# Kernel tuning notes

Measured on AMD Instinct MI355X. Metric: run time of the kernel, lower is better.

## Reference

```python
import jax, jax.numpy as jnp
import numpy as np

EPS_W = 1e-8   # weight reciprocal eps (matches torch code)
EPS_BN = 1e-5  # torch BatchNorm1d default eps


def _cdist(a, b):
    # a: [B,N,3], b: [B,M,3] -> [B,N,M] euclidean distances
    sq = (jnp.sum(a * a, -1)[:, :, None] + jnp.sum(b * b, -1)[:, None, :]
          - 2.0 * jnp.einsum('bnd,bmd->bnm', a, b))
    return jnp.sqrt(jnp.maximum(sq, 0.0))


def _bn_relu(x, gamma, beta):
    # x: [B,C,N]; training-mode batch norm over (B,N)
    mean = jnp.mean(x, axis=(0, 2), keepdims=True)
    var = jnp.mean((x - mean) ** 2, axis=(0, 2), keepdims=True)
    y = (x - mean) * jax.lax.rsqrt(var + EPS_BN)
    y = y * gamma[None, :, None] + beta[None, :, None]
    return jax.nn.relu(y)


def setup_inputs() -> dict:
    key = jax.random.key(0)
    ks = jax.random.split(key, 8)
    B, Np, Ns = 16, 1024, 4096
    Cp, Cs, Co = 256, 128, 256
    return {
        'xyz_prev': jax.random.normal(ks[0], (B, Np, 3), jnp.float32),
        'xyz_skip': jax.random.normal(ks[1], (B, Ns, 3), jnp.float32),
        'points_prev': jax.random.normal(ks[2], (B, Cp, Np), jnp.float32),
        'points_skip': jax.random.normal(ks[3], (B, Cs, Ns), jnp.float32),
        'W1': jax.random.normal(ks[4], (Co, Cp + Cs), jnp.float32) * 0.05,
        'g1': jnp.ones((Co,), jnp.float32),
        'b1': jnp.zeros((Co,), jnp.float32),
        'W2': jax.random.normal(ks[5], (Co, Co), jnp.float32) * 0.05,
        'g2': jnp.ones((Co,), jnp.float32),
        'b2': jnp.zeros((Co,), jnp.float32),
    }


def reference(xyz_prev, xyz_skip, points_prev, points_skip, W1, g1, b1, W2, g2, b2):
    dist = _cdist(xyz_skip, xyz_prev)                       # [B,Ns,Np]
    neg, idx = jax.lax.top_k(-dist, 3)                      # 3 smallest dists
    dist_recip = 1.0 / (dist + EPS_W)
    # NOTE: normalization is over ALL N_prev points (faithful to source)
    weight = dist_recip / jnp.sum(dist_recip, axis=2, keepdims=True)
    w3 = jnp.take_along_axis(weight, idx, axis=2)           # [B,Ns,3]
    pp = jnp.swapaxes(points_prev, 1, 2)                    # [B,Np,Cp]
    g = jnp.take_along_axis(pp[:, None, :, :], idx[..., None], axis=2)  # [B,Ns,3,Cp]
    interp = jnp.einsum('bnk,bnkc->bcn', w3, g)             # [B,Cp,Ns]
    x = jnp.concatenate([interp, points_skip], axis=1)      # [B,Cp+Cs,Ns]
    x = _bn_relu(jnp.einsum('bcn,oc->bon', x, W1), g1, b1)
    x = _bn_relu(jnp.einsum('bcn,oc->bon', x, W2), g2, b2)
    return x
```

## Files before the change

kernel.cpp:

```cpp
#include <hip/hip_runtime.h>
#include <math.h>

constexpr int NB  = 16;
constexpr int NP  = 1024;
constexpr int NS  = 4096;
constexpr int CP  = 256;
constexpr int CS  = 128;
constexpr int CIN = 384;
constexpr int CO  = 256;

constexpr int NCHUNK = 16;
constexpr int CHPTS  = NP / NCHUNK;

typedef unsigned int uint;
typedef unsigned short ushort_t;
typedef __attribute__((ext_vector_type(8))) short short8;
typedef __attribute__((ext_vector_type(4))) float f32x4;

__device__ __forceinline__ ushort_t f2bf(float f) {
  uint u = __float_as_uint(f);
  uint r = (u + 0x7fffu + ((u >> 16) & 1u)) >> 16;
  return (ushort_t)r;
}
__device__ __forceinline__ float bf2f(ushort_t u) {
  return __uint_as_float(((uint)u) << 16);
}
__device__ __forceinline__ uint pk2(ushort_t lo, ushort_t hi) {
  return (uint)lo | ((uint)hi << 16);
}

__device__ __forceinline__ void gload16(const void* g, void* l) {
  __builtin_amdgcn_global_load_lds(
      (const __attribute__((address_space(1))) uint*)g,
      (__attribute__((address_space(3))) uint*)l, 16, 0, 0);
}

__device__ __forceinline__ void tkp(float pxv, float pyv, float pzv, int pi,
                                    float qx, float qy, float qz,
                                    float& k0, float& k1, float& k2,
                                    float& rsum) {
  float dx = pxv - qx, dy = pyv - qy, dz = pzv - qz;
  float sq = fmaf(dz, dz, fmaf(dy, dy, fmaf(dx, dx, 1e-16f)));
  rsum += __builtin_amdgcn_rsqf(sq);
  float k = __uint_as_float((__float_as_uint(sq) & 0xFFFFFC00u) | (uint)pi);
  k2 = __builtin_amdgcn_fmed3f(k1, k2, k);
  k1 = __builtin_amdgcn_fmed3f(k0, k1, k);
  k0 = fminf(k0, k);
}

__global__ __launch_bounds__(256) void topk_chunk_kernel(
    const float* __restrict__ xyz_prev, const float* __restrict__ xyz_skip,
    float* __restrict__ pbuf) {
  __shared__ float px[CHPTS], py[CHPTS], pz[CHPTS];
  int q  = blockIdx.y;
  int b  = blockIdx.z;
  int tid = threadIdx.x;
  if (tid < CHPTS) {
    const float* xp = xyz_prev + ((size_t)b * NP + q * CHPTS + tid) * 3;
    px[tid] = xp[0]; py[tid] = xp[1]; pz[tid] = xp[2];
  }
  __syncthreads();
  int nA = blockIdx.x * 512 + tid;
  int nB = nA + 256;
  const float* xqA = xyz_skip + ((size_t)b * NS + nA) * 3;
  const float* xqB = xyz_skip + ((size_t)b * NS + nB) * 3;
  float qxA = xqA[0], qyA = xqA[1], qzA = xqA[2];
  float qxB = xqB[0], qyB = xqB[1], qzB = xqB[2];
  float kA0 = INFINITY, kA1 = INFINITY, kA2 = INFINITY;
  float kB0 = INFINITY, kB1 = INFINITY, kB2 = INFINITY;
  float rsA = 0.f, rsB = 0.f;
  int pbase = q * CHPTS;

  for (int p = 0; p < CHPTS; p += 4) {
    float4 X = *(const float4*)&px[p];
    float4 Y = *(const float4*)&py[p];
    float4 Z = *(const float4*)&pz[p];
    tkp(X.x, Y.x, Z.x, pbase + p + 0, qxA, qyA, qzA, kA0, kA1, kA2, rsA);
    tkp(X.x, Y.x, Z.x, pbase + p + 0, qxB, qyB, qzB, kB0, kB1, kB2, rsB);
    tkp(X.y, Y.y, Z.y, pbase + p + 1, qxA, qyA, qzA, kA0, kA1, kA2, rsA);
    tkp(X.y, Y.y, Z.y, pbase + p + 1, qxB, qyB, qzB, kB0, kB1, kB2, rsB);
    tkp(X.z, Y.z, Z.z, pbase + p + 2, qxA, qyA, qzA, kA0, kA1, kA2, rsA);
    tkp(X.z, Y.z, Z.z, pbase + p + 2, qxB, qyB, qzB, kB0, kB1, kB2, rsB);
    tkp(X.w, Y.w, Z.w, pbase + p + 3, qxA, qyA, qzA, kA0, kA1, kA2, rsA);
    tkp(X.w, Y.w, Z.w, pbase + p + 3, qxB, qyB, qzB, kB0, kB1, kB2, rsB);
  }

  size_t PA = ((size_t)(b * NCHUNK + q) * NS + nA) * 4;
  size_t PB = ((size_t)(b * NCHUNK + q) * NS + nB) * 4;
  *(float4*)(pbuf + PA) = make_float4(kA0, kA1, kA2, rsA);
  *(float4*)(pbuf + PB) = make_float4(kB0, kB1, kB2, rsB);
}

__global__ __launch_bounds__(256) void topk_merge_kernel(
    const float* __restrict__ pbuf, float* __restrict__ w3,
    int* __restrict__ idx3) {
  int gid = blockIdx.x * 256 + threadIdx.x;
  int b = gid >> 12;
  int n = gid & (NS - 1);
  float k0 = INFINITY, k1 = INFINITY, k2 = INFINITY;
  float rsum = 0.f;
  #pragma unroll 4
  for (int q = 0; q < NCHUNK; q++) {
    float4 v = *(const float4*)(pbuf + ((size_t)(b * NCHUNK + q) * NS + n) * 4);
    rsum += v.w;
    k2 = __builtin_amdgcn_fmed3f(k1, k2, v.x);
    k1 = __builtin_amdgcn_fmed3f(k0, k1, v.x);
    k0 = fminf(k0, v.x);
    k2 = __builtin_amdgcn_fmed3f(k1, k2, v.y);
    k1 = __builtin_amdgcn_fmed3f(k0, k1, v.y);
    k0 = fminf(k0, v.y);
    k2 = __builtin_amdgcn_fmed3f(k1, k2, v.z);
    k1 = __builtin_amdgcn_fmed3f(k0, k1, v.z);
    k0 = fminf(k0, v.z);
  }
  float inv = 1.0f / rsum;
  uint u0 = __float_as_uint(k0), u1 = __float_as_uint(k1), u2 = __float_as_uint(k2);
  float d0 = __uint_as_float(u0 & 0xFFFFFC00u);
  float d1 = __uint_as_float(u1 & 0xFFFFFC00u);
  float d2 = __uint_as_float(u2 & 0xFFFFFC00u);
  size_t base = (size_t)gid * 3;
  w3[base + 0] = __builtin_amdgcn_rsqf(d0) * inv;
  w3[base + 1] = __builtin_amdgcn_rsqf(d1) * inv;
  w3[base + 2] = __builtin_amdgcn_rsqf(d2) * inv;
  idx3[base + 0] = (int)(u0 & 1023u);
  idx3[base + 1] = (int)(u1 & 1023u);
  idx3[base + 2] = (int)(u2 & 1023u);
}

__global__ __launch_bounds__(256) void wcast_kernel(
    const float* __restrict__ W1, const float* __restrict__ W2,
    ushort_t* __restrict__ W1b, ushort_t* __restrict__ W2b,
    float* __restrict__ st1, float* __restrict__ st2) {
  int tid = threadIdx.x;
  if (blockIdx.x == 0) {
    st1[tid] = 0.f; st1[tid + 256] = 0.f;
    st2[tid] = 0.f; st2[tid + 256] = 0.f;
  }
  int t = blockIdx.x * 256 + tid;
  int n1 = CO * CIN / 4;
  if (t < n1) {
    float4 v = *(const float4*)(W1 + t * 4);
    ushort4 o; o.x = f2bf(v.x); o.y = f2bf(v.y); o.z = f2bf(v.z); o.w = f2bf(v.w);
    *(ushort4*)(W1b + t * 4) = o;
  } else {
    int u = t - n1;
    float4 v = *(const float4*)(W2 + u * 4);
    ushort4 o; o.x = f2bf(v.x); o.y = f2bf(v.y); o.z = f2bf(v.z); o.w = f2bf(v.w);
    *(ushort4*)(W2b + u * 4) = o;
  }
}

__global__ __launch_bounds__(256) void ppT_kernel(
    const float* __restrict__ pp, ushort_t* __restrict__ pptT) {
  __shared__ float tl[64][65];
  int p0 = blockIdx.x * 64, c0 = blockIdx.y * 64, b = blockIdx.z;
  int tid = threadIdx.x;
  const float* P = pp + (size_t)b * CP * NP;
  int pi4 = (tid & 15) * 4, ci = tid >> 4;
  #pragma unroll
  for (int r = 0; r < 4; r++) {
    int cc = ci + 16 * r;
    float4 v = *(const float4*)(P + (size_t)(c0 + cc) * NP + p0 + pi4);
    tl[cc][pi4] = v.x; tl[cc][pi4 + 1] = v.y; tl[cc][pi4 + 2] = v.z; tl[cc][pi4 + 3] = v.w;
  }
  __syncthreads();
  ushort_t* O = pptT + (size_t)b * NP * CP;
  int ci4 = (tid & 15) * 4, pi = tid >> 4;
  #pragma unroll
  for (int r = 0; r < 4; r++) {
    int pr = pi + 16 * r;
    ushort4 o;
    o.x = f2bf(tl[ci4 + 0][pr]); o.y = f2bf(tl[ci4 + 1][pr]);
    o.z = f2bf(tl[ci4 + 2][pr]); o.w = f2bf(tl[ci4 + 3][pr]);
    *(ushort4*)(O + (size_t)(p0 + pr) * CP + c0 + ci4) = o;
  }
}

__global__ __launch_bounds__(256) void skipT_kernel(
    const float* __restrict__ sk, ushort_t* __restrict__ x1) {
  __shared__ float tl[64][65];
  int n0 = blockIdx.x * 64, c0 = blockIdx.y * 64, b = blockIdx.z;
  int tid = threadIdx.x;
  const float* S = sk + (size_t)b * CS * NS;
  int ni4 = (tid & 15) * 4, ci = tid >> 4;
  #pragma unroll
  for (int r = 0; r < 4; r++) {
    int cc = ci + 16 * r;
    float4 v = *(const float4*)(S + (size_t)(c0 + cc) * NS + n0 + ni4);
    tl[cc][ni4] = v.x; tl[cc][ni4 + 1] = v.y; tl[cc][ni4 + 2] = v.z; tl[cc][ni4 + 3] = v.w;
  }
  __syncthreads();
  ushort_t* O = x1 + (size_t)b * NS * CIN;
  int ci4 = (tid & 15) * 4, ni = tid >> 4;
  #pragma unroll
  for (int r = 0; r < 4; r++) {
    int nr = ni + 16 * r;
    ushort4 o;
    o.x = f2bf(tl[ci4 + 0][nr]); o.y = f2bf(tl[ci4 + 1][nr]);
    o.z = f2bf(tl[ci4 + 2][nr]); o.w = f2bf(tl[ci4 + 3][nr]);
    *(ushort4*)(O + (size_t)(n0 + nr) * CIN + CP + c0 + ci4) = o;
  }
}

__global__ __launch_bounds__(256) void interp_kernel(
    const ushort_t* __restrict__ pptT, const float* __restrict__ w3,
    const int* __restrict__ idx3, ushort_t* __restrict__ x1) {
  int tid = threadIdx.x;
  int nl = tid >> 6, l = tid & 63;
  int b = blockIdx.y;
  int n = blockIdx.x * 4 + nl;
  size_t nb = (size_t)b * NS + n;
  int j0 = idx3[nb * 3 + 0], j1 = idx3[nb * 3 + 1], j2 = idx3[nb * 3 + 2];
  float w0 = w3[nb * 3 + 0], w1 = w3[nb * 3 + 1], w2 = w3[nb * 3 + 2];
  const ushort_t* P = pptT + (size_t)b * NP * CP;
  int c = l * 4;
  ushort4 g0 = *(const ushort4*)(P + (size_t)j0 * CP + c);
  ushort4 g1 = *(const ushort4*)(P + (size_t)j1 * CP + c);
  ushort4 g2 = *(const ushort4*)(P + (size_t)j2 * CP + c);
  ushort4 o;
  o.x = f2bf(w0 * bf2f(g0.x) + w1 * bf2f(g1.x) + w2 * bf2f(g2.x));
  o.y = f2bf(w0 * bf2f(g0.y) + w1 * bf2f(g1.y) + w2 * bf2f(g2.y));
  o.z = f2bf(w0 * bf2f(g0.z) + w1 * bf2f(g1.z) + w2 * bf2f(g2.z));
  o.w = f2bf(w0 * bf2f(g0.w) + w1 * bf2f(g1.w) + w2 * bf2f(g2.w));
  *(ushort4*)(x1 + nb * CIN + c) = o;
}

template <int KD, bool ACT>
__global__ __launch_bounds__(256) void gemm_mfma_kernel(
    const ushort_t* __restrict__ X, const ushort_t* __restrict__ Wb,
    const float* __restrict__ stats_in, const float* __restrict__ g_in,
    const float* __restrict__ bt_in,
    ushort_t* __restrict__ Yb, float* __restrict__ stats) {
  __shared__ ushort_t ldsX[128 * 32];
  __shared__ ushort_t ldsW[128 * 32];
  __shared__ float ssum[128], ssq[128];
  __shared__ float a1s[ACT ? CO : 1], s1s[ACT ? CO : 1];
  int tid = threadIdx.x;
  int w = tid >> 6, l = tid & 63;
  int bid = blockIdx.x;
  int by = (bid >> 3) & 1;
  int s  = (bid & 7) + 8 * (bid >> 4);
  int bx = s & 31;
  int bz = s >> 5;
  int n0 = bx * 128;
  if (tid < 128) { ssum[tid] = 0.f; ssq[tid] = 0.f; }
  if constexpr (ACT) {
    float cnt = (float)NB * (float)NS;
    float m = stats_in[tid] / cnt;
    float var = stats_in[CO + tid] / cnt - m * m;
    var = fmaxf(var, 0.f);
    float invs = rsqrtf(var + 1e-5f);
    float av = g_in[tid] * invs;
    a1s[tid] = av; s1s[tid] = bt_in[tid] - m * av;
  }
  __syncthreads();

  f32x4 acc[4][4];
  #pragma unroll
  for (int i = 0; i < 4; i++)
    #pragma unroll
    for (int j = 0; j < 4; j++) acc[i][j] = {0.f, 0.f, 0.f, 0.f};

  int wn = (w & 1) * 64, wo = (w >> 1) * 64;
  int lr = l & 15, lk = l >> 4;
  const ushort_t* Xb = X + (size_t)bz * NS * KD;
  int rbase = w * 16 + (l >> 2);
  int cl = l & 3;
  int ksw = 8 * (cl ^ ((rbase >> 1) & 3));

  for (int kt = 0; kt < KD / 32; kt++) {
    int k0 = kt * 32;
    int ks = k0 + ksw;
    #pragma unroll
    for (int q = 0; q < 2; q++) {
      int r = q * 64 + rbase;
      gload16(Wb + (size_t)(by * 128 + r) * KD + ks, &ldsW[(q * 64 + w * 16) * 32]);
    }
    if constexpr (!ACT) {
      #pragma unroll
      for (int q = 0; q < 2; q++) {
        int r = q * 64 + rbase;
        gload16(Xb + (size_t)(n0 + r) * KD + ks, &ldsX[(q * 64 + w * 16) * 32]);
      }
    } else {
      float4 av0 = *(const float4*)&a1s[ks];
      float4 av1 = *(const float4*)&a1s[ks + 4];
      float4 sv0 = *(const float4*)&s1s[ks];
      float4 sv1 = *(const float4*)&s1s[ks + 4];
      #pragma unroll
      for (int q = 0; q < 2; q++) {
        int r = q * 64 + rbase;
        const ushort_t* src = Xb + (size_t)(n0 + r) * KD + ks;
        ushort4 v0 = *(const ushort4*)(src);
        ushort4 v1 = *(const ushort4*)(src + 4);
        int4 o;
        o.x = (int)pk2(f2bf(fmaxf(fmaf(av0.x, bf2f(v0.x), sv0.x), 0.f)),
                       f2bf(fmaxf(fmaf(av0.y, bf2f(v0.y), sv0.y), 0.f)));
        o.y = (int)pk2(f2bf(fmaxf(fmaf(av0.z, bf2f(v0.z), sv0.z), 0.f)),
                       f2bf(fmaxf(fmaf(av0.w, bf2f(v0.w), sv0.w), 0.f)));
        o.z = (int)pk2(f2bf(fmaxf(fmaf(av1.x, bf2f(v1.x), sv1.x), 0.f)),
                       f2bf(fmaxf(fmaf(av1.y, bf2f(v1.y), sv1.y), 0.f)));
        o.w = (int)pk2(f2bf(fmaxf(fmaf(av1.z, bf2f(v1.z), sv1.z), 0.f)),
                       f2bf(fmaxf(fmaf(av1.w, bf2f(v1.w), sv1.w), 0.f)));
        *(int4*)&ldsX[(q * 64 + w * 16) * 32 + l * 8] = o;
      }
    }
    __syncthreads();
    short8 a[4], bfr[4];
    #pragma unroll
    for (int i = 0; i < 4; i++) {
      int rr = wn + i * 16 + lr;
      int cs = lk ^ ((rr >> 1) & 3);
      a[i] = *(const short8*)&ldsX[rr * 32 + cs * 8];
    }
    #pragma unroll
    for (int j = 0; j < 4; j++) {
      int rr = wo + j * 16 + lr;
      int cs = lk ^ ((rr >> 1) & 3);
      bfr[j] = *(const short8*)&ldsW[rr * 32 + cs * 8];
    }
    #pragma unroll
    for (int i = 0; i < 4; i++)
      #pragma unroll
      for (int j = 0; j < 4; j++)
        acc[i][j] = __builtin_amdgcn_mfma_f32_16x16x32_bf16(a[i], bfr[j], acc[i][j], 0, 0, 0);
    __syncthreads();
  }

  #pragma unroll
  for (int j = 0; j < 4; j++) {
    int ol = wo + j * 16 + lr;
    int og = by * 128 + ol;
    float ps = 0.f, pq = 0.f;
    #pragma unroll
    for (int i = 0; i < 4; i++) {
      #pragma unroll
      for (int rg = 0; rg < 4; rg++) {
        float v = acc[i][j][rg];
        ps += v; pq += v * v;
        int n = n0 + wn + i * 16 + lk * 4 + rg;
        Yb[((size_t)bz * NS + n) * CO + og] = f2bf(v);
      }
    }
    atomicAdd(&ssum[ol], ps);
    atomicAdd(&ssq[ol], pq);
  }
  __syncthreads();
  if (tid < 128) {
    atomicAdd(&stats[by * 128 + tid], ssum[tid]);
    atomicAdd(&stats[CO + by * 128 + tid], ssq[tid]);
  }
}

__global__ __launch_bounds__(256) void bnrelu_tr_kernel(
    const ushort_t* __restrict__ y2b, const float* __restrict__ stats_in,
    const float* __restrict__ g_in, const float* __restrict__ bt_in,
    float* __restrict__ out) {
  __shared__ float tl[64][65];
  __shared__ float a2s[64], s2s[64];
  int n0 = blockIdx.x * 64, o0 = blockIdx.y * 64, b = blockIdx.z;
  const ushort_t* Y = y2b + (size_t)b * NS * CO;
  int tid = threadIdx.x;
  if (tid < 64) {
    int o = o0 + tid;
    float cnt = (float)NB * (float)NS;
    float m = stats_in[o] / cnt;
    float var = stats_in[CO + o] / cnt - m * m;
    var = fmaxf(var, 0.f);
    float invs = rsqrtf(var + 1e-5f);
    float av = g_in[o] * invs;
    a2s[tid] = av; s2s[tid] = bt_in[o] - m * av;
  }
  int o8 = (tid & 7) * 8, row = tid >> 3;
  #pragma unroll
  for (int r = 0; r < 2; r++) {
    int ii = row + 32 * r;
    const ushort_t* src = Y + (size_t)(n0 + ii) * CO + o0 + o8;
    ushort4 v0 = *(const ushort4*)(src);
    ushort4 v1 = *(const ushort4*)(src + 4);
    tl[ii][o8 + 0] = bf2f(v0.x); tl[ii][o8 + 1] = bf2f(v0.y);
    tl[ii][o8 + 2] = bf2f(v0.z); tl[ii][o8 + 3] = bf2f(v0.w);
    tl[ii][o8 + 4] = bf2f(v1.x); tl[ii][o8 + 5] = bf2f(v1.y);
    tl[ii][o8 + 6] = bf2f(v1.z); tl[ii][o8 + 7] = bf2f(v1.w);
  }
  __syncthreads();
  float* O = out + (size_t)b * CO * NS;
  int ii4 = (tid & 15) * 4, j = tid >> 4;
  #pragma unroll
  for (int r = 0; r < 4; r++) {
    int jj = j + 16 * r;
    float av = a2s[jj], sv = s2s[jj];
    float4 v;
    v.x = fmaxf(fmaf(av, tl[ii4 + 0][jj], sv), 0.f);
    v.y = fmaxf(fmaf(av, tl[ii4 + 1][jj], sv), 0.f);
    v.z = fmaxf(fmaf(av, tl[ii4 + 2][jj], sv), 0.f);
    v.w = fmaxf(fmaf(av, tl[ii4 + 3][jj], sv), 0.f);
    *(float4*)(O + (size_t)(o0 + jj) * NS + n0 + ii4) = v;
  }
}

extern "C" void kernel_launch(void* const* d_in, const int* in_sizes, int n_in,
                              void* d_out, int out_size, void* d_ws, size_t ws_size,
                              hipStream_t stream) {
  const float* xyz_prev    = (const float*)d_in[0];
  const float* xyz_skip    = (const float*)d_in[1];
  const float* points_prev = (const float*)d_in[2];
  const float* points_skip = (const float*)d_in[3];
  const float* W1 = (const float*)d_in[4];
  const float* g1 = (const float*)d_in[5];
  const float* b1 = (const float*)d_in[6];
  const float* W2 = (const float*)d_in[7];
  const float* g2 = (const float*)d_in[8];
  const float* b2 = (const float*)d_in[9];
  float* out = (float*)d_out;

  char* W = (char*)d_ws;
  size_t off = 0;
  auto alloc = [&](size_t bytes) {
    size_t o = off; off = (off + bytes + 255) & ~(size_t)255; return o;
  };
  ushort_t* x1   = (ushort_t*)(W + alloc((size_t)NB * NS * CIN * 2));
  ushort_t* y1b  = (ushort_t*)(W + alloc((size_t)NB * NS * CO * 2));
  ushort_t* pptT = (ushort_t*)(W + alloc((size_t)NB * NP * CP * 2));
  ushort_t* W1b  = (ushort_t*)(W + alloc((size_t)CO * CIN * 2));
  ushort_t* W2b  = (ushort_t*)(W + alloc((size_t)CO * CO * 2));
  float* w3   = (float*)(W + alloc((size_t)NB * NS * 3 * 4));
  int*   idx3 = (int*)(W + alloc((size_t)NB * NS * 3 * 4));
  float* st1  = (float*)(W + alloc(512 * 4));
  float* st2  = (float*)(W + alloc(512 * 4));
  size_t y2_off = alloc((size_t)NB * NS * CO * 2);
  bool full = (ws_size >= off);
  ushort_t* y2b = full ? (ushort_t*)(W + y2_off) : (ushort_t*)d_out;
  float* pbuf = full ? (float*)(W + y2_off) : (float*)d_out;

  hipLaunchKernelGGL(topk_chunk_kernel, dim3(NS / 512, NCHUNK, NB), dim3(256), 0,
                     stream, xyz_prev, xyz_skip, pbuf);
  hipLaunchKernelGGL(topk_merge_kernel, dim3(NB * NS / 256), dim3(256), 0, stream,
                     pbuf, w3, idx3);
  hipLaunchKernelGGL(wcast_kernel, dim3((CO * CIN / 4 + CO * CO / 4 + 255) / 256),
                     dim3(256), 0, stream, W1, W2, W1b, W2b, st1, st2);
  hipLaunchKernelGGL(ppT_kernel, dim3(NP / 64, CP / 64, NB), dim3(256), 0, stream,
                     points_prev, pptT);
  hipLaunchKernelGGL(skipT_kernel, dim3(NS / 64, CS / 64, NB), dim3(256), 0, stream,
                     points_skip, x1);
  hipLaunchKernelGGL(interp_kernel, dim3(NS / 4, NB), dim3(256), 0, stream,
                     pptT, w3, idx3, x1);
  hipLaunchKernelGGL((gemm_mfma_kernel<CIN, false>), dim3(1024), dim3(256),
                     0, stream, x1, W1b, (const float*)nullptr,
                     (const float*)nullptr, (const float*)nullptr, y1b, st1);
  hipLaunchKernelGGL((gemm_mfma_kernel<CO, true>), dim3(1024), dim3(256),
                     0, stream, y1b, W2b, st1, g1, b1, y2b, st2);
  if (full) {
    hipLaunchKernelGGL(bnrelu_tr_kernel, dim3(NS / 64, CO / 64, NB), dim3(256), 0,
                       stream, y2b, st2, g2, b2, out);
  } else {
    float* stage = (float*)d_ws;
    hipLaunchKernelGGL(bnrelu_tr_kernel, dim3(NS / 64, CO / 64, NB), dim3(256), 0,
                       stream, y2b, st2, g2, b2, stage);
    hipMemcpyAsync(out, stage, (size_t)NB * NS * CO * 4, hipMemcpyDeviceToDevice,
                   stream);
  }
}
```

Before: 157.9 us.

## Fuse interpolation gather into first GEMM and pipeline operand loads

Removes the separate interp kernel: the first GEMM now gathers three neighbour rows from the transposed prev features, blends them with the weights in registers and writes the bf16 tile into LDS. Skip features go to a compact buffer instead of the wide concatenated x1. Both GEMMs get register-prefetched X loads and double-buffered W tiles with manual waitcnt and barriers, plus an LDS-staged epilogue that writes coalesced 16-byte output rows. The aim is to cut the x1 write/read round trip and an extra launch, and to overlap loads with MFMA work. In exchange the GEMM does gather work inline and uses more registers, which may lower occupancy.

```diff
diff --git a/kernel.cpp b/kernel.cpp
--- a/kernel.cpp
+++ b/kernel.cpp
@@ -15,6 +15,7 @@
 typedef unsigned int uint;
 typedef unsigned short ushort_t;
 typedef __attribute__((ext_vector_type(8))) short short8;
+typedef __attribute__((ext_vector_type(8))) unsigned short us8;
 typedef __attribute__((ext_vector_type(4))) float f32x4;
 
 __device__ __forceinline__ ushort_t f2bf(float f) {
@@ -24,9 +25,6 @@
 }
 __device__ __forceinline__ float bf2f(ushort_t u) {
   return __uint_as_float(((uint)u) << 16);
-}
-__device__ __forceinline__ uint pk2(ushort_t lo, ushort_t hi) {
-  return (uint)lo | ((uint)hi << 16);
 }
 
 __device__ __forceinline__ void gload16(const void* g, void* l) {
@@ -70,7 +68,6 @@
   float kB0 = INFINITY, kB1 = INFINITY, kB2 = INFINITY;
   float rsA = 0.f, rsB = 0.f;
   int pbase = q * CHPTS;
-
   for (int p = 0; p < CHPTS; p += 4) {
     float4 X = *(const float4*)&px[p];
     float4 Y = *(const float4*)&py[p];
@@ -84,7 +81,6 @@
     tkp(X.w, Y.w, Z.w, pbase + p + 3, qxA, qyA, qzA, kA0, kA1, kA2, rsA);
     tkp(X.w, Y.w, Z.w, pbase + p + 3, qxB, qyB, qzB, kB0, kB1, kB2, rsB);
   }
-
   size_t PA = ((size_t)(b * NCHUNK + q) * NS + nA) * 4;
   size_t PB = ((size_t)(b * NCHUNK + q) * NS + nB) * 4;
   *(float4*)(pbuf + PA) = make_float4(kA0, kA1, kA2, rsA);
@@ -177,7 +173,7 @@
 }
 
 __global__ __launch_bounds__(256) void skipT_kernel(
-    const float* __restrict__ sk, ushort_t* __restrict__ x1) {
+    const float* __restrict__ sk, ushort_t* __restrict__ xsk) {
   __shared__ float tl[64][65];
   int n0 = blockIdx.x * 64, c0 = blockIdx.y * 64, b = blockIdx.z;
   int tid = threadIdx.x;
@@ -190,7 +186,7 @@
     tl[cc][ni4] = v.x; tl[cc][ni4 + 1] = v.y; tl[cc][ni4 + 2] = v.z; tl[cc][ni4 + 3] = v.w;
   }
   __syncthreads();
-  ushort_t* O = x1 + (size_t)b * NS * CIN;
+  ushort_t* O = xsk + (size_t)b * NS * CS;
   int ci4 = (tid & 15) * 4, ni = tid >> 4;
   #pragma unroll
   for (int r = 0; r < 4; r++) {
@@ -198,43 +194,27 @@
     ushort4 o;
     o.x = f2bf(tl[ci4 + 0][nr]); o.y = f2bf(tl[ci4 + 1][nr]);
     o.z = f2bf(tl[ci4 + 2][nr]); o.w = f2bf(tl[ci4 + 3][nr]);
-    *(ushort4*)(O + (size_t)(n0 + nr) * CIN + CP + c0 + ci4) = o;
-  }
-}
-
-__global__ __launch_bounds__(256) void interp_kernel(
-    const ushort_t* __restrict__ pptT, const float* __restrict__ w3,
-    const int* __restrict__ idx3, ushort_t* __restrict__ x1) {
-  int tid = threadIdx.x;
-  int nl = tid >> 6, l = tid & 63;
-  int b = blockIdx.y;
-  int n = blockIdx.x * 4 + nl;
-  size_t nb = (size_t)b * NS + n;
-  int j0 = idx3[nb * 3 + 0], j1 = idx3[nb * 3 + 1], j2 = idx3[nb * 3 + 2];
-  float w0 = w3[nb * 3 + 0], w1 = w3[nb * 3 + 1], w2 = w3[nb * 3 + 2];
-  const ushort_t* P = pptT + (size_t)b * NP * CP;
-  int c = l * 4;
-  ushort4 g0 = *(const ushort4*)(P + (size_t)j0 * CP + c);
-  ushort4 g1 = *(const ushort4*)(P + (size_t)j1 * CP + c);
-  ushort4 g2 = *(const ushort4*)(P + (size_t)j2 * CP + c);
-  ushort4 o;
-  o.x = f2bf(w0 * bf2f(g0.x) + w1 * bf2f(g1.x) + w2 * bf2f(g2.x));
-  o.y = f2bf(w0 * bf2f(g0.y) + w1 * bf2f(g1.y) + w2 * bf2f(g2.y));
-  o.z = f2bf(w0 * bf2f(g0.z) + w1 * bf2f(g1.z) + w2 * bf2f(g2.z));
-  o.w = f2bf(w0 * bf2f(g0.w) + w1 * bf2f(g1.w) + w2 * bf2f(g2.w));
-  *(ushort4*)(x1 + nb * CIN + c) = o;
-}
-
-template <int KD, bool ACT>
-__global__ __launch_bounds__(256) void gemm_mfma_kernel(
-    const ushort_t* __restrict__ X, const ushort_t* __restrict__ Wb,
+    *(ushort4*)(O + (size_t)(n0 + nr) * CS + c0 + ci4) = o;
+  }
+}
+
+template <int MODE>
+__global__ __launch_bounds__(256) void gemm_fused_kernel(
+    const ushort_t* __restrict__ Xsrc,
+    const ushort_t* __restrict__ xsk,
+    const float* __restrict__ w3, const int* __restrict__ idx3,
+    const ushort_t* __restrict__ Wb, ushort_t* __restrict__ Yb,
+    float* __restrict__ stats,
     const float* __restrict__ stats_in, const float* __restrict__ g_in,
-    const float* __restrict__ bt_in,
-    ushort_t* __restrict__ Yb, float* __restrict__ stats) {
-  __shared__ ushort_t ldsX[128 * 32];
-  __shared__ ushort_t ldsW[128 * 32];
+    const float* __restrict__ bt_in) {
+  constexpr int KD = (MODE == 0) ? CIN : CO;
+  constexpr int NT = KD / 32;
+  __shared__ __align__(16) char lds_raw[33792];
+  ushort_t* ldsX = (ushort_t*)lds_raw;
+  ushort_t* ldsW = (ushort_t*)(lds_raw + 8192);
   __shared__ float ssum[128], ssq[128];
-  __shared__ float a1s[ACT ? CO : 1], s1s[ACT ? CO : 1];
+  __shared__ float a1s[MODE ? CO : 1], s1s[MODE ? CO : 1];
+
   int tid = threadIdx.x;
   int w = tid >> 6, l = tid & 63;
   int bid = blockIdx.x;
@@ -244,7 +224,7 @@
   int bz = s >> 5;
   int n0 = bx * 128;
   if (tid < 128) { ssum[tid] = 0.f; ssq[tid] = 0.f; }
-  if constexpr (ACT) {
+  if constexpr (MODE == 1) {
     float cnt = (float)NB * (float)NS;
     float m = stats_in[tid] / cnt;
     float var = stats_in[CO + tid] / cnt - m * m;
@@ -255,6 +235,53 @@
   }
   __syncthreads();
 
+  int r = tid >> 1, h = tid & 1;
+  int sw = (r >> 1) & 3;
+  int p0c = 2 * h, p1c = 2 * h + 1;
+  int cl0 = (p0c ^ sw) * 8, cl1 = (p1c ^ sw) * 8;
+  int j0 = 0, j1 = 0, j2 = 0; float w0 = 0.f, w1 = 0.f, w2 = 0.f;
+  const ushort_t* Pb = nullptr; const ushort_t* Kb = nullptr;
+  const ushort_t* Xb = nullptr;
+  if constexpr (MODE == 0) {
+    size_t nb3 = ((size_t)bz * NS + n0 + r) * 3;
+    j0 = idx3[nb3 + 0]; j1 = idx3[nb3 + 1]; j2 = idx3[nb3 + 2];
+    w0 = w3[nb3 + 0]; w1 = w3[nb3 + 1]; w2 = w3[nb3 + 2];
+    Pb = Xsrc + (size_t)bz * NP * CP;
+    Kb = xsk + ((size_t)bz * NS + n0 + r) * CS;
+  } else {
+    Xb = Xsrc + ((size_t)bz * NS + n0 + r) * KD;
+  }
+  int wrb = w * 16 + (l >> 2);
+  int wcl = l & 3;
+  int wksw = 8 * (wcl ^ ((wrb >> 1) & 3));
+
+  us8 ra0, rb0, rc0, ra1, rb1, rc1;
+  us8 rg0, rg1;
+
+  auto issue = [&](int tt) {
+    int cb = tt * 32;
+    if constexpr (MODE == 0) {
+      if (cb < CP) {
+        ra0 = *(const us8*)(Pb + (size_t)j0 * CP + cb + cl0);
+        rb0 = *(const us8*)(Pb + (size_t)j1 * CP + cb + cl0);
+        rc0 = *(const us8*)(Pb + (size_t)j2 * CP + cb + cl0);
+        ra1 = *(const us8*)(Pb + (size_t)j0 * CP + cb + cl1);
+        rb1 = *(const us8*)(Pb + (size_t)j1 * CP + cb + cl1);
+        rc1 = *(const us8*)(Pb + (size_t)j2 * CP + cb + cl1);
+      } else {
+        rg0 = *(const us8*)(Kb + cb - CP + cl0);
+        rg1 = *(const us8*)(Kb + cb - CP + cl1);
+      }
+    } else {
+      rg0 = *(const us8*)(Xb + cb + cl0);
+      rg1 = *(const us8*)(Xb + cb + cl1);
+    }
+    ushort_t* wdst = ldsW + (tt & 1) * (128 * 32);
+    int ks = cb + wksw;
+    gload16(Wb + (size_t)(by * 128 + wrb) * KD + ks, &wdst[(w * 16) * 32]);
+    gload16(Wb + (size_t)(by * 128 + 64 + wrb) * KD + ks, &wdst[(64 + w * 16) * 32]);
+  };
+
   f32x4 acc[4][4];
   #pragma unroll
   for (int i = 0; i < 4; i++)
@@ -263,89 +290,111 @@
 
   int wn = (w & 1) * 64, wo = (w >> 1) * 64;
   int lr = l & 15, lk = l >> 4;
-  const ushort_t* Xb = X + (size_t)bz * NS * KD;
-  int rbase = w * 16 + (l >> 2);
-  int cl = l & 3;
-  int ksw = 8 * (cl ^ ((rbase >> 1) & 3));
-
-  for (int kt = 0; kt < KD / 32; kt++) {
-    int k0 = kt * 32;
-    int ks = k0 + ksw;
-    #pragma unroll
-    for (int q = 0; q < 2; q++) {
-      int r = q * 64 + rbase;
-      gload16(Wb + (size_t)(by * 128 + r) * KD + ks, &ldsW[(q * 64 + w * 16) * 32]);
+
+  issue(0);
+
+  #pragma unroll
+  for (int t = 0; t < NT; t++) {
+    {
+      us8 v0, v1;
+      if constexpr (MODE == 0) {
+        if (t * 32 < CP) {
+          #pragma unroll
+          for (int e = 0; e < 8; e++) {
+            v0[e] = f2bf(w0 * bf2f(ra0[e]) + w1 * bf2f(rb0[e]) + w2 * bf2f(rc0[e]));
+            v1[e] = f2bf(w0 * bf2f(ra1[e]) + w1 * bf2f(rb1[e]) + w2 * bf2f(rc1[e]));
+          }
+        } else { v0 = rg0; v1 = rg1; }
+      } else {
+        int c0l = t * 32 + cl0, c1l = t * 32 + cl1;
+        float4 a0 = *(const float4*)&a1s[c0l], a0b = *(const float4*)&a1s[c0l + 4];
+        float4 s0 = *(const float4*)&s1s[c0l], s0b = *(const float4*)&s1s[c0l + 4];
+        float4 a1v = *(const float4*)&a1s[c1l], a1b = *(const float4*)&a1s[c1l + 4];
+        float4 s1v = *(const float4*)&s1s[c1l], s1b = *(const float4*)&s1s[c1l + 4];
+        const float* a0p = (const float*)&a0; const float* a0bp = (const float*)&a0b;
+        const float* s0p = (const float*)&s0; const float* s0bp = (const float*)&s0b;
+        const float* a1p = (const float*)&a1v; const float* a1bp = (const float*)&a1b;
+        const float* s1p = (const float*)&s1v; const float* s1bp = (const float*)&s1b;
+        #pragma unroll
+        for (int e = 0; e < 4; e++) {
+          v0[e]     = f2bf(fmaxf(fmaf(a0p[e],  bf2f(rg0[e]),     s0p[e]),  0.f));
+          v0[e + 4] = f2bf(fmaxf(fmaf(a0bp[e], bf2f(rg0[e + 4]), s0bp[e]), 0.f));
+          v1[e]     = f2bf(fmaxf(fmaf(a1p[e],  bf2f(rg1[e]),     s1p[e]),  0.f));
+          v1[e + 4] = f2bf(fmaxf(fmaf(a1bp[e], bf2f(rg1[e + 4]), s1bp[e]), 0.f));
+        }
+      }
+      *(us8*)&ldsX[r * 32 + p0c * 8] = v0;
+      *(us8*)&ldsX[r * 32 + p1c * 8] = v1;
     }
-    if constexpr (!ACT) {
+    if (t + 1 < NT) issue(t + 1);
+    if constexpr (MODE == 0) {
+      if (t + 1 < 8)        asm volatile("s_waitcnt vmcnt(8) lgkmcnt(0)" ::: "memory");
+      else if (t + 1 < NT)  asm volatile("s_waitcnt vmcnt(4) lgkmcnt(0)" ::: "memory");
+      else                  asm volatile("s_waitcnt vmcnt(0) lgkmcnt(0)" ::: "memory");
+    } else {
+      if (t + 1 < NT)       asm volatile("s_waitcnt vmcnt(4) lgkmcnt(0)" ::: "memory");
+      else                  asm volatile("s_waitcnt vmcnt(0) lgkmcnt(0)" ::: "memory");
+    }
+    __builtin_amdgcn_s_barrier();
+    __builtin_amdgcn_sched_barrier(0);
+    {
+      const ushort_t* Wl = ldsW + (t & 1) * (128 * 32);
+      short8 af[4], bf_[4];
       #pragma unroll
-      for (int q = 0; q < 2; q++) {
-        int r = q * 64 + rbase;
-        gload16(Xb + (size_t)(n0 + r) * KD + ks, &ldsX[(q * 64 + w * 16) * 32]);
+      for (int i = 0; i < 4; i++) {
+        int rr = wn + i * 16 + lr;
+        int cs = lk ^ ((rr >> 1) & 3);
+        af[i] = *(const short8*)&ldsX[rr * 32 + cs * 8];
       }
-    } else {
-      float4 av0 = *(const float4*)&a1s[ks];
-      float4 av1 = *(const float4*)&a1s[ks + 4];
-      float4 sv0 = *(const float4*)&s1s[ks];
-      float4 sv1 = *(const float4*)&s1s[ks + 4];
       #pragma unroll
-      for (int q = 0; q < 2; q++) {
-        int r = q * 64 + rbase;
-        const ushort_t* src = Xb + (size_t)(n0 + r) * KD + ks;
-        ushort4 v0 = *(const ushort4*)(src);
-        ushort4 v1 = *(const ushort4*)(src + 4);
-        int4 o;
-        o.x = (int)pk2(f2bf(fmaxf(fmaf(av0.x, bf2f(v0.x), sv0.x), 0.f)),
-                       f2bf(fmaxf(fmaf(av0.y, bf2f(v0.y), sv0.y), 0.f)));
-        o.y = (int)pk2(f2bf(fmaxf(fmaf(av0.z, bf2f(v0.z), sv0.z), 0.f)),
-                       f2bf(fmaxf(fmaf(av0.w, bf2f(v0.w), sv0.w), 0.f)));
-        o.z = (int)pk2(f2bf(fmaxf(fmaf(av1.x, bf2f(v1.x), sv1.x), 0.f)),
-                       f2bf(fmaxf(fmaf(av1.y, bf2f(v1.y), sv1.y), 0.f)));
-        o.w = (int)pk2(f2bf(fmaxf(fmaf(av1.z, bf2f(v1.z), sv1.z), 0.f)),
-                       f2bf(fmaxf(fmaf(av1.w, bf2f(v1.w), sv1.w), 0.f)));
-        *(int4*)&ldsX[(q * 64 + w * 16) * 32 + l * 8] = o;
+      for (int j = 0; j < 4; j++) {
+        int rr = wo + j * 16 + lr;
+        int cs = lk ^ ((rr >> 1) & 3);
+        bf_[j] = *(const short8*)&Wl[rr * 32 + cs * 8];
       }
+      __builtin_amdgcn_s_setprio(1);
+      #pragma unroll
+      for (int i = 0; i < 4; i++)
+        #pragma unroll
+        for (int j = 0; j < 4; j++)
+          acc[i][j] = __builtin_amdgcn_mfma_f32_16x16x32_bf16(af[i], bf_[j], acc[i][j], 0, 0, 0);
+      __builtin_amdgcn_s_setprio(0);
     }
-    __syncthreads();
-    short8 a[4], bfr[4];
-    #pragma unroll
-    for (int i = 0; i < 4; i++) {
-      int rr = wn + i * 16 + lr;
-      int cs = lk ^ ((rr >> 1) & 3);
-      a[i] = *(const short8*)&ldsX[rr * 32 + cs * 8];
-    }
-    #pragma unroll
-    for (int j = 0; j < 4; j++) {
-      int rr = wo + j * 16 + lr;
-      int cs = lk ^ ((rr >> 1) & 3);
-      bfr[j] = *(const short8*)&ldsW[rr * 32 + cs * 8];
-    }
+    __builtin_amdgcn_s_barrier();
+    __builtin_amdgcn_sched_barrier(0);
+  }
+
+  #pragma unroll
+  for (int j = 0; j < 4; j++) {
+    int ol = wo + j * 16 + lr;
+    float ps = 0.f, pq = 0.f;
     #pragma unroll
     for (int i = 0; i < 4; i++)
       #pragma unroll
-      for (int j = 0; j < 4; j++)
-        acc[i][j] = __builtin_amdgcn_mfma_f32_16x16x32_bf16(a[i], bfr[j], acc[i][j], 0, 0, 0);
-    __syncthreads();
-  }
-
-  #pragma unroll
-  for (int j = 0; j < 4; j++) {
-    int ol = wo + j * 16 + lr;
-    int og = by * 128 + ol;
-    float ps = 0.f, pq = 0.f;
+      for (int rg = 0; rg < 4; rg++) { float v = acc[i][j][rg]; ps += v; pq += v * v; }
+    atomicAdd(&ssum[ol], ps);
+    atomicAdd(&ssq[ol], pq);
+  }
+  ushort_t* lout = (ushort_t*)lds_raw;
+  #pragma unroll
+  for (int i = 0; i < 4; i++)
     #pragma unroll
-    for (int i = 0; i < 4; i++) {
+    for (int j = 0; j < 4; j++)
       #pragma unroll
       for (int rg = 0; rg < 4; rg++) {
-        float v = acc[i][j][rg];
-        ps += v; pq += v * v;
-        int n = n0 + wn + i * 16 + lk * 4 + rg;
-        Yb[((size_t)bz * NS + n) * CO + og] = f2bf(v);
+        int nl = wn + i * 16 + lk * 4 + rg;
+        int ol = wo + j * 16 + lr;
+        lout[nl * 132 + ol] = f2bf(acc[i][j][rg]);
       }
-    }
-    atomicAdd(&ssum[ol], ps);
-    atomicAdd(&ssq[ol], pq);
-  }
   __syncthreads();
+  {
+    int row = tid >> 1, half = tid & 1;
+    const ushort_t* src = lout + row * 132 + half * 64;
+    ushort_t* dst = Yb + ((size_t)bz * NS + n0 + row) * CO + by * 128 + half * 64;
+    #pragma unroll
+    for (int k = 0; k < 8; k++)
+      *(us8*)(dst + k * 8) = *(const us8*)(src + k * 8);
+  }
   if (tid < 128) {
     atomicAdd(&stats[by * 128 + tid], ssum[tid]);
     atomicAdd(&stats[CO + by * 128 + tid], ssq[tid]);
@@ -419,7 +468,7 @@
   auto alloc = [&](size_t bytes) {
     size_t o = off; off = (off + bytes + 255) & ~(size_t)255; return o;
   };
-  ushort_t* x1   = (ushort_t*)(W + alloc((size_t)NB * NS * CIN * 2));
+  ushort_t* xsk  = (ushort_t*)(W + alloc((size_t)NB * NS * CS * 2));
   ushort_t* y1b  = (ushort_t*)(W + alloc((size_t)NB * NS * CO * 2));
   ushort_t* pptT = (ushort_t*)(W + alloc((size_t)NB * NP * CP * 2));
   ushort_t* W1b  = (ushort_t*)(W + alloc((size_t)CO * CIN * 2));
@@ -442,14 +491,14 @@
   hipLaunchKernelGGL(ppT_kernel, dim3(NP / 64, CP / 64, NB), dim3(256), 0, stream,
                      points_prev, pptT);
   hipLaunchKernelGGL(skipT_kernel, dim3(NS / 64, CS / 64, NB), dim3(256), 0, stream,
-                     points_skip, x1);
-  hipLaunchKernelGGL(interp_kernel, dim3(NS / 4, NB), dim3(256), 0, stream,
-                     pptT, w3, idx3, x1);
-  hipLaunchKernelGGL((gemm_mfma_kernel<CIN, false>), dim3(1024), dim3(256),
-                     0, stream, x1, W1b, (const float*)nullptr,
-                     (const float*)nullptr, (const float*)nullptr, y1b, st1);
-  hipLaunchKernelGGL((gemm_mfma_kernel<CO, true>), dim3(1024), dim3(256),
-                     0, stream, y1b, W2b, st1, g1, b1, y2b, st2);
+                     points_skip, xsk);
+  hipLaunchKernelGGL((gemm_fused_kernel<0>), dim3(1024), dim3(256), 0, stream,
+                     pptT, xsk, w3, idx3, W1b, y1b, st1,
+                     (const float*)nullptr, (const float*)nullptr,
+                     (const float*)nullptr);
+  hipLaunchKernelGGL((gemm_fused_kernel<1>), dim3(1024), dim3(256), 0, stream,
+                     y1b, (const ushort_t*)nullptr, (const float*)nullptr,
+                     (const int*)nullptr, W2b, y2b, st2, st1, g1, b1);
   if (full) {
     hipLaunchKernelGGL(bnrelu_tr_kernel, dim3(NS / 64, CO / 64, NB), dim3(256), 0,
                        stream, y2b, st2, g2, b2, out);
```

After: 160.3 us. Within noise of the previous version (+1.6%).

## Widen GEMM K-tile to 64 and stage bf16 output through LDS for coalesced stores

Applied to the files above, without the earlier changes.

Both MFMA GEMMs now load 64-wide K tiles with an XOR-swizzled LDS layout, which halves the number of barrier-separated iterations. The MFMA loop is wrapped in s_setprio, and launch bounds now request 4 blocks per SM. The epilogue writes the accumulators into a padded LDS tile, then copies each row back with 16-byte vector stores, replacing the scattered 2-byte global stores. LDS use per block rises to about 33 KB, which may reduce occupancy.

```diff
diff --git a/kernel.cpp b/kernel.cpp
--- a/kernel.cpp
+++ b/kernel.cpp
@@ -15,6 +15,7 @@
 typedef unsigned int uint;
 typedef unsigned short ushort_t;
 typedef __attribute__((ext_vector_type(8))) short short8;
+typedef __attribute__((ext_vector_type(8))) unsigned short us8;
 typedef __attribute__((ext_vector_type(4))) float f32x4;
 
 __device__ __forceinline__ ushort_t f2bf(float f) {
@@ -24,9 +25,6 @@
 }
 __device__ __forceinline__ float bf2f(ushort_t u) {
   return __uint_as_float(((uint)u) << 16);
-}
-__device__ __forceinline__ uint pk2(ushort_t lo, ushort_t hi) {
-  return (uint)lo | ((uint)hi << 16);
 }
 
 __device__ __forceinline__ void gload16(const void* g, void* l) {
@@ -70,7 +68,6 @@
   float kB0 = INFINITY, kB1 = INFINITY, kB2 = INFINITY;
   float rsA = 0.f, rsB = 0.f;
   int pbase = q * CHPTS;
-
   for (int p = 0; p < CHPTS; p += 4) {
     float4 X = *(const float4*)&px[p];
     float4 Y = *(const float4*)&py[p];
@@ -84,7 +81,6 @@
     tkp(X.w, Y.w, Z.w, pbase + p + 3, qxA, qyA, qzA, kA0, kA1, kA2, rsA);
     tkp(X.w, Y.w, Z.w, pbase + p + 3, qxB, qyB, qzB, kB0, kB1, kB2, rsB);
   }
-
   size_t PA = ((size_t)(b * NCHUNK + q) * NS + nA) * 4;
   size_t PB = ((size_t)(b * NCHUNK + q) * NS + nB) * 4;
   *(float4*)(pbuf + PA) = make_float4(kA0, kA1, kA2, rsA);
@@ -225,26 +221,29 @@
   *(ushort4*)(x1 + nb * CIN + c) = o;
 }
 
-template <int KD, bool ACT>
-__global__ __launch_bounds__(256) void gemm_mfma_kernel(
+template <int MODE>
+__global__ __launch_bounds__(256, 4) void gemm_bk64_kernel(
     const ushort_t* __restrict__ X, const ushort_t* __restrict__ Wb,
+    ushort_t* __restrict__ Yb, float* __restrict__ stats,
     const float* __restrict__ stats_in, const float* __restrict__ g_in,
-    const float* __restrict__ bt_in,
-    ushort_t* __restrict__ Yb, float* __restrict__ stats) {
-  __shared__ ushort_t ldsX[128 * 32];
-  __shared__ ushort_t ldsW[128 * 32];
+    const float* __restrict__ bt_in) {
+  constexpr int KD = MODE ? CO : CIN;
+  constexpr int NT = KD / 64;
+  __shared__ __align__(16) char lds_raw[33792];
+  ushort_t* ldsX = (ushort_t*)lds_raw;
+  ushort_t* ldsW = (ushort_t*)(lds_raw + 16384);
   __shared__ float ssum[128], ssq[128];
-  __shared__ float a1s[ACT ? CO : 1], s1s[ACT ? CO : 1];
+  __shared__ float a1s[MODE ? CO : 1], s1s[MODE ? CO : 1];
+
   int tid = threadIdx.x;
   int w = tid >> 6, l = tid & 63;
   int bid = blockIdx.x;
   int by = (bid >> 3) & 1;
-  int s  = (bid & 7) + 8 * (bid >> 4);
-  int bx = s & 31;
-  int bz = s >> 5;
+  int s = (bid & 7) + 8 * (bid >> 4);
+  int bx = s & 31, bz = s >> 5;
   int n0 = bx * 128;
   if (tid < 128) { ssum[tid] = 0.f; ssq[tid] = 0.f; }
-  if constexpr (ACT) {
+  if constexpr (MODE == 1) {
     float cnt = (float)NB * (float)NS;
     float m = stats_in[tid] / cnt;
     float var = stats_in[CO + tid] / cnt - m * m;
@@ -255,6 +254,12 @@
   }
   __syncthreads();
 
+  int grow = l >> 3;
+  int glc  = (l & 7) ^ grow;
+  int trow = tid >> 3;
+  int tlc  = (tid & 7) ^ (trow & 7);
+  const ushort_t* Xb = X + (size_t)bz * NS * KD;
+
   f32x4 acc[4][4];
   #pragma unroll
   for (int i = 0; i < 4; i++)
@@ -263,89 +268,94 @@
 
   int wn = (w & 1) * 64, wo = (w >> 1) * 64;
   int lr = l & 15, lk = l >> 4;
-  const ushort_t* Xb = X + (size_t)bz * NS * KD;
-  int rbase = w * 16 + (l >> 2);
-  int cl = l & 3;
-  int ksw = 8 * (cl ^ ((rbase >> 1) & 3));
-
-  for (int kt = 0; kt < KD / 32; kt++) {
-    int k0 = kt * 32;
-    int ks = k0 + ksw;
-    #pragma unroll
-    for (int q = 0; q < 2; q++) {
-      int r = q * 64 + rbase;
-      gload16(Wb + (size_t)(by * 128 + r) * KD + ks, &ldsW[(q * 64 + w * 16) * 32]);
+
+  for (int t = 0; t < NT; t++) {
+    int k0 = t * 64;
+    #pragma unroll
+    for (int i = 0; i < 4; i++) {
+      int row = w * 32 + i * 8 + grow;
+      gload16(Wb + (size_t)(by * 128 + row) * KD + k0 + glc * 8,
+              &ldsW[(w * 32 + i * 8) * 64]);
     }
-    if constexpr (!ACT) {
-      #pragma unroll
-      for (int q = 0; q < 2; q++) {
-        int r = q * 64 + rbase;
-        gload16(Xb + (size_t)(n0 + r) * KD + ks, &ldsX[(q * 64 + w * 16) * 32]);
+    if constexpr (MODE == 0) {
+      #pragma unroll
+      for (int i = 0; i < 4; i++) {
+        int row = w * 32 + i * 8 + grow;
+        gload16(Xb + (size_t)(n0 + row) * KD + k0 + glc * 8,
+                &ldsX[(w * 32 + i * 8) * 64]);
       }
     } else {
-      float4 av0 = *(const float4*)&a1s[ks];
-      float4 av1 = *(const float4*)&a1s[ks + 4];
-      float4 sv0 = *(const float4*)&s1s[ks];
-      float4 sv1 = *(const float4*)&s1s[ks + 4];
-      #pragma unroll
-      for (int q = 0; q < 2; q++) {
-        int r = q * 64 + rbase;
-        const ushort_t* src = Xb + (size_t)(n0 + r) * KD + ks;
-        ushort4 v0 = *(const ushort4*)(src);
-        ushort4 v1 = *(const ushort4*)(src + 4);
-        int4 o;
-        o.x = (int)pk2(f2bf(fmaxf(fmaf(av0.x, bf2f(v0.x), sv0.x), 0.f)),
-                       f2bf(fmaxf(fmaf(av0.y, bf2f(v0.y), sv0.y), 0.f)));
-        o.y = (int)pk2(f2bf(fmaxf(fmaf(av0.z, bf2f(v0.z), sv0.z), 0.f)),
-                       f2bf(fmaxf(fmaf(av0.w, bf2f(v0.w), sv0.w), 0.f)));
-        o.z = (int)pk2(f2bf(fmaxf(fmaf(av1.x, bf2f(v1.x), sv1.x), 0.f)),
-                       f2bf(fmaxf(fmaf(av1.y, bf2f(v1.y), sv1.y), 0.f)));
-        o.w = (int)pk2(f2bf(fmaxf(fmaf(av1.z, bf2f(v1.z), sv1.z), 0.f)),
-                       f2bf(fmaxf(fmaf(av1.w, bf2f(v1.w), sv1.w), 0.f)));
-        *(int4*)&ldsX[(q * 64 + w * 16) * 32 + l * 8] = o;
+      #pragma unroll
+      for (int c = 0; c < 4; c++) {
+        int row = trow + 32 * c;
+        us8 v = *(const us8*)(Xb + (size_t)(n0 + row) * KD + k0 + tlc * 8);
+        const float* ap = &a1s[k0 + tlc * 8];
+        const float* sp = &s1s[k0 + tlc * 8];
+        us8 o;
+        #pragma unroll
+        for (int e = 0; e < 8; e++)
+          o[e] = f2bf(fmaxf(fmaf(ap[e], bf2f(v[e]), sp[e]), 0.f));
+        *(us8*)&ldsX[(tid + 256 * c) * 8] = o;
       }
     }
     __syncthreads();
-    short8 a[4], bfr[4];
-    #pragma unroll
-    for (int i = 0; i < 4; i++) {
-      int rr = wn + i * 16 + lr;
-      int cs = lk ^ ((rr >> 1) & 3);
-      a[i] = *(const short8*)&ldsX[rr * 32 + cs * 8];
+    #pragma unroll
+    for (int ks = 0; ks < 2; ks++) {
+      short8 af[4], bfr[4];
+      #pragma unroll
+      for (int i = 0; i < 4; i++) {
+        int rr = wn + i * 16 + lr;
+        int pc = (ks * 4 + lk) ^ (rr & 7);
+        af[i] = *(const short8*)&ldsX[rr * 64 + pc * 8];
+      }
+      #pragma unroll
+      for (int j = 0; j < 4; j++) {
+        int rr = wo + j * 16 + lr;
+        int pc = (ks * 4 + lk) ^ (rr & 7);
+        bfr[j] = *(const short8*)&ldsW[rr * 64 + pc * 8];
+      }
+      __builtin_amdgcn_s_setprio(1);
+      #pragma unroll
+      for (int i = 0; i < 4; i++)
+        #pragma unroll
+        for (int j = 0; j < 4; j++)
+          acc[i][j] = __builtin_amdgcn_mfma_f32_16x16x32_bf16(af[i], bfr[j], acc[i][j], 0, 0, 0);
+      __builtin_amdgcn_s_setprio(0);
     }
-    #pragma unroll
-    for (int j = 0; j < 4; j++) {
-      int rr = wo + j * 16 + lr;
-      int cs = lk ^ ((rr >> 1) & 3);
-      bfr[j] = *(const short8*)&ldsW[rr * 32 + cs * 8];
-    }
-    #pragma unroll
-    for (int i = 0; i < 4; i++)
-      #pragma unroll
-      for (int j = 0; j < 4; j++)
-        acc[i][j] = __builtin_amdgcn_mfma_f32_16x16x32_bf16(a[i], bfr[j], acc[i][j], 0, 0, 0);
     __syncthreads();
   }
 
   #pragma unroll
   for (int j = 0; j < 4; j++) {
     int ol = wo + j * 16 + lr;
-    int og = by * 128 + ol;
     float ps = 0.f, pq = 0.f;
     #pragma unroll
-    for (int i = 0; i < 4; i++) {
-      #pragma unroll
-      for (int rg = 0; rg < 4; rg++) {
-        float v = acc[i][j][rg];
-        ps += v; pq += v * v;
-        int n = n0 + wn + i * 16 + lk * 4 + rg;
-        Yb[((size_t)bz * NS + n) * CO + og] = f2bf(v);
-      }
-    }
+    for (int i = 0; i < 4; i++)
+      #pragma unroll
+      for (int rg = 0; rg < 4; rg++) { float v = acc[i][j][rg]; ps += v; pq += v * v; }
     atomicAdd(&ssum[ol], ps);
     atomicAdd(&ssq[ol], pq);
   }
-  __syncthreads();
+  ushort_t* lout = (ushort_t*)lds_raw;
+  #pragma unroll
+  for (int i = 0; i < 4; i++)
+    #pragma unroll
+    for (int j = 0; j < 4; j++)
+      #pragma unroll
+      for (int rg = 0; rg < 4; rg++) {
+        int nl = wn + i * 16 + lk * 4 + rg;
+        int ol = wo + j * 16 + lr;
+        lout[nl * 132 + ol] = f2bf(acc[i][j][rg]);
+      }
+  __syncthreads();
+  {
+    int row = tid >> 1, half = tid & 1;
+    const ushort_t* src = lout + row * 132 + half * 64;
+    ushort_t* dst = Yb + ((size_t)bz * NS + n0 + row) * CO + by * 128 + half * 64;
+    #pragma unroll
+    for (int k = 0; k < 8; k++)
+      *(us8*)(dst + k * 8) = *(const us8*)(src + k * 8);
+  }
   if (tid < 128) {
     atomicAdd(&stats[by * 128 + tid], ssum[tid]);
     atomicAdd(&stats[CO + by * 128 + tid], ssq[tid]);
@@ -445,11 +455,11 @@
                      points_skip, x1);
   hipLaunchKernelGGL(interp_kernel, dim3(NS / 4, NB), dim3(256), 0, stream,
                      pptT, w3, idx3, x1);
-  hipLaunchKernelGGL((gemm_mfma_kernel<CIN, false>), dim3(1024), dim3(256),
-                     0, stream, x1, W1b, (const float*)nullptr,
-                     (const float*)nullptr, (const float*)nullptr, y1b, st1);
-  hipLaunchKernelGGL((gemm_mfma_kernel<CO, true>), dim3(1024), dim3(256),
-                     0, stream, y1b, W2b, st1, g1, b1, y2b, st2);
+  hipLaunchKernelGGL((gemm_bk64_kernel<0>), dim3(1024), dim3(256), 0, stream,
+                     x1, W1b, y1b, st1, (const float*)nullptr,
+                     (const float*)nullptr, (const float*)nullptr);
+  hipLaunchKernelGGL((gemm_bk64_kernel<1>), dim3(1024), dim3(256), 0, stream,
+                     y1b, W2b, y2b, st2, st1, g1, b1);
   if (full) {
     hipLaunchKernelGGL(bnrelu_tr_kernel, dim3(NS / 64, CO / 64, NB), dim3(256), 0,
                        stream, y2b, st2, g2, b2, out);
```

Result: slower. 165.8 us (+5.1%).
